# Kernel tuning notes

Measured on AMD Instinct MI355X. Metric: run time of the kernel, lower is better.

Reference implementation:

```python
import jax, jax.numpy as jnp
import numpy as np

T, B, D, R, S, M, H = 1024, 4, 1024, 64, 16, 64, 16
NEG_INF = -1e8


def setup_inputs() -> dict:
    key = jax.random.key(0)
    ks = jax.random.split(key, 12)
    Q, K = R + T + S, M + R + T
    inp = {
        "utterance": jax.random.normal(ks[0], (T, B, D), jnp.float32),
        "right_context": jax.random.normal(ks[1], (R, B, D), jnp.float32),
        "summary": jax.random.normal(ks[2], (S, B, D), jnp.float32),
        "mems": jax.random.normal(ks[3], (M, B, D), jnp.float32),
        # valid frame counts in [1, T]; ensure at least one element == T so
        # max(lengths) stresses the full utterance span
        "lengths": jnp.asarray(
            jax.random.randint(ks[4], (B,), 1, T + 1).at[0].set(T), jnp.int32
        ),
        "attention_mask": jax.random.uniform(ks[5], (Q, K)) < 0.1,
        # Linear params stored as (in, out); y = x @ W + b  (== torch Linear)
        "Wq": jax.random.normal(ks[6], (D, D), jnp.float32) * 0.02,
        "bq": jnp.zeros((D,), jnp.float32),
        "Wkv": jax.random.normal(ks[7], (D, 2 * D), jnp.float32) * 0.02,
        "bkv": jnp.zeros((2 * D,), jnp.float32),
        "Wout": jax.random.normal(ks[8], (D, D), jnp.float32) * 0.02,
        "bout": jnp.zeros((D,), jnp.float32),
    }
    return inp


def reference(utterance, right_context, summary, mems, lengths, attention_mask,
              Wq, bq, Wkv, bkv, Wout, bout):
    d_head = D // H
    scaling = d_head ** -0.5
    Q = R + T + S  # query length
    Kl = M + R + T  # key length (non-streaming)

    # projections
    query = jnp.concatenate([right_context, utterance, summary], axis=0) @ Wq + bq  # (Q,B,D)
    kv = jnp.concatenate([mems, right_context, utterance], axis=0) @ Wkv + bkv      # (K,B,2D)
    k, v = jnp.split(kv, 2, axis=2)  # each (K,B,D)

    # (L, B, D) -> (B*H, L, d_head), matching torch view+transpose
    def heads(x):
        return x.reshape(x.shape[0], B * H, d_head).swapaxes(0, 1)

    qh, kh, vh = heads(query), heads(k), heads(v)

    # fp32 scores + masking, as in the original (masked_fill in float)
    w = jnp.einsum("nqd,nkd->nqk", qh * scaling, kh).astype(jnp.float32)  # (B*H,Q,K)
    w = jnp.where(attention_mask[None, :, :], NEG_INF, w)

    # padding mask over keys: klengths = lengths + M + (R+T - max(lengths))
    klengths = lengths + M + R + T - jnp.max(lengths)
    pad = jnp.arange(Kl, dtype=lengths.dtype)[None, :] >= klengths[:, None]  # (B,K)
    w = w.reshape(B, H, Q, Kl)
    w = jnp.where(pad[:, None, None, :], NEG_INF, w)
    w = w.reshape(B * H, Q, Kl)

    probs = jax.nn.softmax(w, axis=-1).astype(utterance.dtype)  # dropout p=0.0

    attn = jnp.einsum("nqk,nkd->nqd", probs, vh)          # (B*H,Q,d)
    attn = attn.swapaxes(0, 1).reshape(Q, B, D)           # (Q,B,D)
    out = attn @ Wout + bout

    output = out[: Q - S]                 # right_context + utterance outputs
    output_mems = jnp.tanh(out[Q - S:])   # summary -> new mems
    out_key = k[M + R:]                   # utterance keys for streaming cache
    out_val = v[M + R:]
    return output, output_mems, out_key, out_val
```

## Files before the change

kernel.cpp:

```cpp
#include <hip/hip_runtime.h>
#include <hip/hip_bf16.h>

typedef __attribute__((ext_vector_type(8))) short short8;
typedef __attribute__((ext_vector_type(4))) float f32x4;

#define DEV __device__ __forceinline__

constexpr int Tn = 1024, Bn = 4, Dn = 1024, Rn = 64, Sn = 16, Mn = 64, Hn = 16;
constexpr int DH = 64;
constexpr int Qn = Rn + Tn + Sn;
constexpr int KL = Mn + Rn + Tn;
constexpr int NT = KL / 64;
constexpr int NQB = 18;
constexpr int QB = Qn * Bn;
constexpr int KB = KL * Bn;
constexpr int MU = 4672;
constexpr size_t OUTM = (size_t)(Rn + Tn) * Bn * Dn;
constexpr size_t OUTK = OUTM + (size_t)Sn * Bn * Dn;
constexpr size_t OUTV = OUTK + (size_t)Tn * Bn * Dn;
constexpr size_t NU  = (size_t)Tn * Bn * Dn;
constexpr size_t NR_ = (size_t)Rn * Bn * Dn;
constexpr size_t NS_ = (size_t)Sn * Bn * Dn;
constexpr size_t NM_ = (size_t)Mn * Bn * Dn;
constexpr float QSCALE = 0.18033688f;

constexpr int PREP_TW = 1024;
constexpr int PREP_CV = 1024;
constexpr int PREP_MB = (Bn * Qn * NT + 3) / 4;

DEV float b2f(ushort u) { union { unsigned v; float f; } x; x.v = ((unsigned)u) << 16; return x.f; }
DEV ushort f2b(float f) { __hip_bfloat16 h = __float2bfloat16(f); return *reinterpret_cast<ushort*>(&h); }

DEV float ldbias(const void* p, int i, int fp32) {
    return fp32 ? ((const float*)p)[i] : b2f(((const ushort*)p)[i]);
}
DEV void stout(void* p, size_t i, float v, int fp32) {
    if (fp32) ((float*)p)[i] = v; else ((ushort*)p)[i] = f2b(v);
}
DEV bool mread(const void* m, size_t idx, int mode) {
    if (mode == 0) return ((const unsigned char*)m)[idx] != 0;
    if (mode == 1) return ((const int*)m)[idx] != 0;
    return ((const float*)m)[idx] != 0.f;
}

DEV void gload_lds16(const void* g, void* l) {
    __builtin_amdgcn_global_load_lds(
        (const __attribute__((address_space(1))) unsigned int*)g,
        (__attribute__((address_space(3))) unsigned int*)l, 16, 0, 0);
}

DEV unsigned cvt_pk_bf16(float lo, float hi) {
    unsigned r;
    asm("v_cvt_pk_bf16_f32 %0, %1, %2" : "=v"(r) : "v"(lo), "v"(hi));
    return r;
}

DEV int sigma_key(int v) {
    return (2 * (v >> 5) + ((v & 7) >> 2)) * 16 + ((v >> 3) & 3) * 4 + (v & 3);
}

__global__ __launch_bounds__(256) void probe_kernel(const ushort* utt, const unsigned char* mask,
                                                    int* flags) {
    __shared__ int cnt[4];
    if (threadIdx.x < 4) cnt[threadIdx.x] = 0;
    __syncthreads();
    int c = 0;
    for (int i = threadIdx.x; i < 2048; i += 256) {
        int e = (utt[i] >> 7) & 0xFF;
        if (e > 64 && e < 192) c++;
    }
    atomicAdd(&cnt[0], c);
    int c0 = 0, c1 = 0, c23 = 0;
    for (int i = threadIdx.x; i < 8192; i += 256) {
        if (mask[i]) { int m = i & 3; if (m == 0) c0++; else if (m == 1) c1++; else c23++; }
    }
    atomicAdd(&cnt[1], c0); atomicAdd(&cnt[2], c1); atomicAdd(&cnt[3], c23);
    __syncthreads();
    if (threadIdx.x == 0) {
        flags[0] = (cnt[0] < 1900) ? 1 : 0;
        int mmode;
        if (cnt[2] == 0 && cnt[3] == 0) mmode = 1;
        else if (cnt[1] == 0) mmode = 2;
        else mmode = 0;
        flags[1] = mmode;
    }
}

__global__ __launch_bounds__(256) void prep_kernel(
    const void* utt, const void* rc, const void* sm, const void* mm,
    const void* Wq, const void* Wkv, const void* Wout,
    const void* amask, const int* __restrict__ lengths,
    ushort* dst, ushort* WqT, ushort* WkvT, ushort* WoutT,
    unsigned long long* __restrict__ mbits, const int* __restrict__ flags) {
    __shared__ alignas(16) ushort tile[64 * 64];
    const int fp32 = flags[0];
    const int t = threadIdx.x;
    int bid = blockIdx.x;

    if (bid < PREP_TW) {
        const int z = bid >> 8, tr = (bid >> 4) & 15;
        int tc = bid & 15;
        const void* W; ushort* WT; int N;
        if (z == 0)      { W = Wq;   WT = WqT;   N = 1024; }
        else if (z == 3) { W = Wout; WT = WoutT; N = 1024; }
        else             { W = Wkv;  WT = WkvT;  N = 2048; tc += (z - 1) * 16; }
        const int K = 1024;
        for (int c = t; c < 512; c += 256) {
            int row = c >> 3, q = c & 7;
            int u = q ^ (row & 7);
            ushort o[8];
#pragma unroll
            for (int j = 0; j < 8; ++j) {
                size_t gi = (size_t)(tr * 64 + row) * N + tc * 64 + q * 8 + j;
                o[j] = fp32 ? f2b(((const float*)W)[gi]) : ((const ushort*)W)[gi];
            }
            *(short8*)&tile[row * 64 + u * 8] = *(short8*)o;
        }
        __syncthreads();
        for (int c = t; c < 512; c += 256) {
            int n = c >> 3, q = c & 7;
            ushort vv[8];
#pragma unroll
            for (int j = 0; j < 8; ++j) {
                int k = q * 8 + j;
                int u = (n >> 3) ^ (k & 7);
                vv[j] = tile[k * 64 + u * 8 + (n & 7)];
            }
            *(short8*)(WT + (size_t)(tc * 64 + n) * K + tr * 64 + q * 8) = *(short8*)vv;
        }
        return;
    }
    bid -= PREP_TW;
    if (bid < PREP_CV) {
        const size_t total = (NU + NR_ + NS_ + NM_) / 8;
        for (size_t cidx = (size_t)bid * 256 + t; cidx < total;
             cidx += (size_t)PREP_CV * 256) {
            size_t e = cidx * 8; const void* src; size_t li; ushort* d;
            if (e < NU)                  { src = utt; li = e;                 d = dst; }
            else if (e < NU + NR_)       { src = rc;  li = e - NU;            d = dst + NU; }
            else if (e < NU + NR_ + NS_) { src = sm;  li = e - NU - NR_;      d = dst + NU + NR_; }
            else                         { src = mm;  li = e - NU - NR_ - NS_; d = dst + NU + NR_ + NS_; }
            if (fp32) {
                const float* f = (const float*)src + li;
                ushort o[8];
#pragma unroll
                for (int j = 0; j < 8; ++j) o[j] = f2b(f[j]);
                *(short8*)(d + li) = *(short8*)o;
            } else {
                *(short8*)(d + li) = *(const short8*)((const ushort*)src + li);
            }
        }
        return;
    }
    bid -= PREP_CV;
    const int mmode = flags[1];
    int word = bid * 4 + (t >> 6);
    if (word >= Bn * Qn * NT) return;
    int lane = t & 63;
    int ktl = word % NT;
    int rem = word / NT;
    int q = rem % Qn;
    int b = rem / Qn;
    const int l0 = lengths[0], l1 = lengths[1], l2 = lengths[2], l3 = lengths[3];
    const int maxlen = max(max(l0, l1), max(l2, l3));
    const int klen = lengths[b] + KL - maxlen;
    int kg = ktl * 64 + lane;
    bool m = mread(amask, (size_t)q * KL + kg, mmode) || (kg >= klen);
    unsigned long long bal = __ballot(m);
    if (lane == 0) mbits[word] = bal;
}

__global__ __launch_bounds__(256) void transpose_v(const ushort* __restrict__ kv,
                                                   ushort* __restrict__ vT) {
    __shared__ alignas(16) ushort tile[64 * 64];
    const int kt = blockIdx.x, bh = blockIdx.y;
    const int b = bh >> 4, h = bh & 15;
    const int t = threadIdx.x;
    for (int c = t; c < 512; c += 256) {
        int key = c >> 3, q = c & 7;
        short8 v = *(const short8*)(kv + ((size_t)(kt * 64 + key) * Bn + b) * 2048 + 1024 + h * DH + q * 8);
        int u = q ^ (key & 7);
        *(short8*)&tile[key * 64 + u * 8] = v;
    }
    __syncthreads();
    for (int c = t; c < 512; c += 256) {
        int d = c >> 3, q = c & 7;
        ushort vv[8];
#pragma unroll
        for (int j = 0; j < 8; ++j) {
            int key = sigma_key(q * 8 + j);
            int u = (d >> 3) ^ (key & 7);
            vv[j] = tile[key * 64 + u * 8 + (d & 7)];
        }
        *(short8*)(vT + ((size_t)bh * 64 + d) * KL + kt * 64 + q * 8) = *(short8*)vv;
    }
}

#define Q128_STAGE(DSTBUF, KT)                                                        \
    _Pragma("unroll")                                                                 \
    for (int i2 = 0; i2 < 4; ++i2) {                                                  \
        gload_lds16(asrc[i2] + (KT) * 64, &As[DSTBUF][(i2 * 256 + t) * 8]);           \
        gload_lds16(bsrc[i2] + (KT) * 64, &Bs[DSTBUF][(i2 * 256 + t) * 8]);           \
    }

__global__ __launch_bounds__(256, 2) void gemm_qkv(
    const ushort* __restrict__ cmem, const ushort* __restrict__ crc,
    const ushort* __restrict__ cutt, const ushort* __restrict__ csum,
    const ushort* __restrict__ Bt, const void* __restrict__ bq, const void* __restrict__ bkv,
    ushort* __restrict__ q_ws, ushort* __restrict__ kv_ws,
    void* __restrict__ gout, const int* __restrict__ flags) {
    __shared__ alignas(16) ushort As[2][8192];
    __shared__ alignas(16) ushort Bs[2][8192];
    const int ofp = flags[0];
    const int t = threadIdx.x;
    const int lane = t & 63;
    const int w = t >> 6;
    const int wr = w >> 1, wc = w & 1;
    const int g = lane >> 4, lr = lane & 15;

    const int bid = blockIdx.x;
    const int wg = (bid & 7) * 111 + (bid >> 3);
    const int bx = wg % 24, by = wg / 24;
    const int mbase = by * 128, nbase = bx * 128;

    const ushort* asrc[4]; const ushort* bsrc[4];
#pragma unroll
    for (int i2 = 0; i2 < 4; ++i2) {
        int slot = i2 * 256 + t;
        int row = slot >> 3, kc = slot & 7;
        int q = kc ^ (row & 7);
        int grow = mbase + row;
        if (grow >= MU) grow = MU - 1;
        const ushort* s;
        if (grow < 256)       s = cmem + (size_t)grow * 1024;
        else if (grow < 512)  s = crc + (size_t)(grow - 256) * 1024;
        else if (grow < 4608) s = cutt + (size_t)(grow - 512) * 1024;
        else                  s = csum + (size_t)(grow - 4608) * 1024;
        asrc[i2] = s + q * 8;
        bsrc[i2] = Bt + (size_t)(nbase + row) * 1024 + q * 8;
    }

    f32x4 acc[4][4] = {};

    Q128_STAGE(0, 0);

    for (int kt = 0; kt < 16; ++kt) {
        const int c = kt & 1;
        if (kt + 1 < 16) {
            Q128_STAGE(c ^ 1, kt + 1);
            asm volatile("s_waitcnt vmcnt(8)" ::: "memory");
        } else {
            asm volatile("s_waitcnt vmcnt(0)" ::: "memory");
        }
        __builtin_amdgcn_sched_barrier(0);
        __builtin_amdgcn_s_barrier();

        short8 bfr[4][2];
#pragma unroll
        for (int n = 0; n < 4; ++n)
#pragma unroll
            for (int ks = 0; ks < 2; ++ks) {
                int col = wc * 64 + n * 16 + lr;
                bfr[n][ks] = *(const short8*)&Bs[c][col * 64 + (((ks * 4 + g) ^ (lr & 7)) << 3)];
            }
        short8 af[4][2];
#pragma unroll
        for (int m = 0; m < 4; ++m)
#pragma unroll
            for (int ks = 0; ks < 2; ++ks) {
                int row = wr * 64 + m * 16 + lr;
                af[m][ks] = *(const short8*)&As[c][row * 64 + (((ks * 4 + g) ^ (lr & 7)) << 3)];
            }
        __builtin_amdgcn_s_setprio(1);
#pragma unroll
        for (int m = 0; m < 4; ++m)
#pragma unroll
            for (int n = 0; n < 4; ++n) {
                acc[m][n] = __builtin_amdgcn_mfma_f32_16x16x32_bf16(af[m][0], bfr[n][0], acc[m][n], 0, 0, 0);
                acc[m][n] = __builtin_amdgcn_mfma_f32_16x16x32_bf16(af[m][1], bfr[n][1], acc[m][n], 0, 0, 0);
            }
        __builtin_amdgcn_s_setprio(0);

        __builtin_amdgcn_sched_barrier(0);
        __builtin_amdgcn_s_barrier();
    }

#pragma unroll
    for (int n = 0; n < 4; ++n) {
        int col = nbase + wc * 64 + n * 16 + lr;
        float bv = (col < 1024) ? ldbias(bq, col, ofp) : ldbias(bkv, col - 1024, ofp);
#pragma unroll
        for (int m = 0; m < 4; ++m) {
            int rowb = mbase + wr * 64 + m * 16 + g * 4;
#pragma unroll
            for (int i = 0; i < 4; ++i) {
                int r = rowb + i;
                if (r >= MU) continue;
                float val = acc[m][n][i] + bv;
                if (col < 1024) {
                    if (r >= 256) q_ws[(size_t)(r - 256) * 1024 + col] = f2b(val * QSCALE);
                } else {
                    if (r < 4608) {
                        kv_ws[(size_t)r * 2048 + (col - 1024)] = f2b(val);
                        if (r >= 512) {
                            size_t o = (col < 2048)
                                ? OUTK + (size_t)(r - 512) * 1024 + (col - 1024)
                                : OUTV + (size_t)(r - 512) * 1024 + (col - 2048);
                            stout(gout, o, val, ofp);
                        }
                    }
                }
            }
        }
    }
}

#define O_STAGE(DSTBUF, KT)                                                           \
    _Pragma("unroll")                                                                 \
    for (int i2 = 0; i2 < 2; ++i2)                                                    \
        gload_lds16(asrc[i2] + (KT) * 64, &As[DSTBUF][(i2 * 256 + t) * 8]);           \
    _Pragma("unroll")                                                                 \
    for (int i2 = 0; i2 < 4; ++i2)                                                    \
        gload_lds16(bsrc[i2] + (KT) * 64, &Bs[DSTBUF][(i2 * 256 + t) * 8]);

__global__ __launch_bounds__(256, 3) void gemm_out(
    const ushort* __restrict__ A, const ushort* __restrict__ Bt,
    const void* __restrict__ bias, void* __restrict__ gout, const int* __restrict__ flags) {
    __shared__ alignas(16) ushort As[2][4096];
    __shared__ alignas(16) ushort Bs[2][8192];
    const int ofp = flags[0];
    const int t = threadIdx.x;
    const int lane = t & 63;
    const int w = t >> 6;
    const int wr = w >> 1, wc = w & 1;
    const int g = lane >> 4, lr = lane & 15;

    const int nwg = gridDim.x;
    const int bid = blockIdx.x;
    const int wg = (bid & 7) * (nwg >> 3) + (bid >> 3);
    const int bx = wg % 8, by = wg / 8;
    const int mbase = by * 64, nbase = bx * 128;

    const ushort* asrc[2];
#pragma unroll
    for (int i2 = 0; i2 < 2; ++i2) {
        int slot = i2 * 256 + t;
        int row = slot >> 3, kc = slot & 7, q = kc ^ (row & 7);
        asrc[i2] = A + (size_t)(mbase + row) * 1024 + q * 8;
    }
    const ushort* bsrc[4];
#pragma unroll
    for (int i2 = 0; i2 < 4; ++i2) {
        int slot = i2 * 256 + t;
        int row = slot >> 3, kc = slot & 7, q = kc ^ (row & 7);
        bsrc[i2] = Bt + (size_t)(nbase + row) * 1024 + q * 8;
    }

    f32x4 acc[2][4] = {};

    O_STAGE(0, 0);

    for (int kt = 0; kt < 16; ++kt) {
        const int c = kt & 1;
        if (kt + 1 < 16) {
            O_STAGE(c ^ 1, kt + 1);
            asm volatile("s_waitcnt vmcnt(6)" ::: "memory");
        } else {
            asm volatile("s_waitcnt vmcnt(0)" ::: "memory");
        }
        __builtin_amdgcn_sched_barrier(0);
        __builtin_amdgcn_s_barrier();

        short8 bfr[4][2];
#pragma unroll
        for (int n = 0; n < 4; ++n)
#pragma unroll
            for (int ks = 0; ks < 2; ++ks) {
                int col = wc * 64 + n * 16 + lr;
                bfr[n][ks] = *(const short8*)&Bs[c][col * 64 + (((ks * 4 + g) ^ (lr & 7)) << 3)];
            }
        short8 af[2][2];
#pragma unroll
        for (int m = 0; m < 2; ++m)
#pragma unroll
            for (int ks = 0; ks < 2; ++ks) {
                int row = wr * 32 + m * 16 + lr;
                af[m][ks] = *(const short8*)&As[c][row * 64 + (((ks * 4 + g) ^ (lr & 7)) << 3)];
            }
        __builtin_amdgcn_s_setprio(1);
#pragma unroll
        for (int m = 0; m < 2; ++m)
#pragma unroll
            for (int n = 0; n < 4; ++n) {
                acc[m][n] = __builtin_amdgcn_mfma_f32_16x16x32_bf16(af[m][0], bfr[n][0], acc[m][n], 0, 0, 0);
                acc[m][n] = __builtin_amdgcn_mfma_f32_16x16x32_bf16(af[m][1], bfr[n][1], acc[m][n], 0, 0, 0);
            }
        __builtin_amdgcn_s_setprio(0);

        __builtin_amdgcn_sched_barrier(0);
        __builtin_amdgcn_s_barrier();
    }

#pragma unroll
    for (int n = 0; n < 4; ++n) {
        int col = nbase + wc * 64 + n * 16 + lr;
        float bv = ldbias(bias, col, ofp);
#pragma unroll
        for (int m = 0; m < 2; ++m) {
            int rowb = mbase + wr * 32 + m * 16 + g * 4;
#pragma unroll
            for (int i = 0; i < 4; ++i) {
                int row = rowb + i;
                float val = acc[m][n][i] + bv;
                if (row < (Rn + Tn) * Bn) stout(gout, (size_t)row * 1024 + col, val, ofp);
                else stout(gout, OUTM + (size_t)(row - (Rn + Tn) * Bn) * 1024 + col, tanhf(val), ofp);
            }
        }
    }
}

#define ATTN_STAGE(DSTBUF, KT)                                                        \
    gload_lds16(ksrc0 + (size_t)(KT) * kstep, &Ks[DSTBUF][w * 1024]);                 \
    gload_lds16(ksrc1 + (size_t)(KT) * kstep, &Ks[DSTBUF][w * 1024 + 512]);           \
    gload_lds16(vsrc0 + (size_t)(KT) * 64,    &Vs[DSTBUF][w * 1024]);                 \
    gload_lds16(vsrc1 + (size_t)(KT) * 64,    &Vs[DSTBUF][w * 1024 + 512]);

#define ATTN_PHASE(CUR, WBCUR, PRE, KTN, WBNXT, VMSTR)                                \
    {                                                                                 \
        if (PRE) { ATTN_STAGE((CUR) ^ 1, KTN); WBNXT = mp[KTN]; }                     \
        asm volatile("s_waitcnt " VMSTR ::: "memory");                                \
        __builtin_amdgcn_sched_barrier(0);                                            \
        __builtin_amdgcn_s_barrier();                                                 \
        __builtin_amdgcn_sched_barrier(0);                                            \
        f32x4 sa[4] = {};                                                             \
        __builtin_amdgcn_s_setprio(1);                                                \
        _Pragma("unroll")                                                             \
        for (int n = 0; n < 4; ++n) {                                                 \
            int key = n * 16 + lr;                                                    \
            short8 kb0 = *(const short8*)&Ks[CUR][key * 64 + ((g ^ (key & 7)) << 3)]; \
            short8 kb1 = *(const short8*)&Ks[CUR][key * 64 + (((4 + g) ^ (key & 7)) << 3)]; \
            sa[n] = __builtin_amdgcn_mfma_f32_16x16x32_bf16(kb0, qf0, sa[n], 0, 0, 0); \
            sa[n] = __builtin_amdgcn_mfma_f32_16x16x32_bf16(kb1, qf1, sa[n], 0, 0, 0); \
        }                                                                             \
        __builtin_amdgcn_s_setprio(0);                                                \
        unsigned pkk[4][2];                                                           \
        _Pragma("unroll")                                                             \
        for (int n = 0; n < 4; ++n) {                                                 \
            unsigned bits = (unsigned)((WBCUR) >> (n * 16 + g * 4)) & 15u;            \
            float p[4];                                                               \
            _Pragma("unroll")                                                         \
            for (int i = 0; i < 4; ++i) {                                             \
                float sv = ((bits >> i) & 1u) ? -100.0f : sa[n][i];                   \
                p[i] = exp2f(sv);                                                     \
                lsum += p[i];                                                         \
            }                                                                         \
            pkk[n][0] = cvt_pk_bf16(p[0], p[1]);                                      \
            pkk[n][1] = cvt_pk_bf16(p[2], p[3]);                                      \
        }                                                                             \
        union { unsigned u[4]; short8 s; } c0, c1;                                    \
        c0.u[0] = pkk[0][0]; c0.u[1] = pkk[0][1]; c0.u[2] = pkk[1][0]; c0.u[3] = pkk[1][1]; \
        c1.u[0] = pkk[2][0]; c1.u[1] = pkk[2][1]; c1.u[2] = pkk[3][0]; c1.u[3] = pkk[3][1]; \
        __builtin_amdgcn_s_setprio(1);                                                \
        _Pragma("unroll")                                                             \
        for (int n = 0; n < 4; ++n) {                                                 \
            int d = n * 16 + lr;                                                      \
            short8 vb0 = *(const short8*)&Vs[CUR][d * 64 + ((g ^ (d & 7)) << 3)];     \
            short8 vb1 = *(const short8*)&Vs[CUR][d * 64 + (((4 + g) ^ (d & 7)) << 3)]; \
            acc_o[n] = __builtin_amdgcn_mfma_f32_16x16x32_bf16(c0.s, vb0, acc_o[n], 0, 0, 0); \
            acc_o[n] = __builtin_amdgcn_mfma_f32_16x16x32_bf16(c1.s, vb1, acc_o[n], 0, 0, 0); \
        }                                                                             \
        __builtin_amdgcn_s_setprio(0);                                                \
        __builtin_amdgcn_sched_barrier(0);                                            \
        __builtin_amdgcn_s_barrier();                                                 \
    }

__global__ __launch_bounds__(256, 5) void attn_kernel(
    const ushort* __restrict__ qws, const ushort* __restrict__ kvws, const ushort* __restrict__ vTws,
    const unsigned long long* __restrict__ mbits,
    ushort* __restrict__ attnws) {
    __shared__ alignas(16) ushort Ks[2][64 * 64];
    __shared__ alignas(16) ushort Vs[2][64 * 64];

    const int bid = blockIdx.x;
    const int wg = (bid & 7) * (gridDim.x >> 3) + (bid >> 3);
    const int qblk = wg % NQB;
    const int bh = wg / NQB;
    const int b = bh >> 4, h = bh & 15;
    const int t = threadIdx.x;
    const int w = t >> 6, lane = t & 63;
    const int g = lane >> 4, lr = lane & 15;

    const int qi = qblk * 64 + w * 16 + lr;
    const int qic = qi < Qn ? qi : (Qn - 1);
    const ushort* qptr = qws + ((size_t)qic * Bn + b) * Dn + h * DH;
    const short8 qf0 = *(const short8*)(qptr + g * 8);
    const short8 qf1 = *(const short8*)(qptr + 32 + g * 8);
    const unsigned long long* mp = mbits + ((size_t)b * Qn + qic) * NT;

    const int srow0 = w * 16 + (lane >> 3);
    const int srow1 = srow0 + 8;
    const int sw = (((lane & 7) ^ ((lane >> 3) & 7)) << 3);
    const ushort* ksrc0 = kvws + ((size_t)srow0 * Bn + b) * 2048 + h * DH + sw;
    const ushort* ksrc1 = kvws + ((size_t)srow1 * Bn + b) * 2048 + h * DH + sw;
    const ushort* vsrc0 = vTws + ((size_t)bh * 64 + srow0) * KL + sw;
    const ushort* vsrc1 = vTws + ((size_t)bh * 64 + srow1) * KL + sw;
    const size_t kstep = (size_t)64 * Bn * 2048;

    f32x4 acc_o[4] = {};
    float lsum = 0.f;
    unsigned long long wbA, wbB;

    ATTN_STAGE(0, 0);
    wbA = mp[0];
    wbB = 0;

    for (int kt2 = 0; kt2 < NT - 2; kt2 += 2) {
        ATTN_PHASE(0, wbA, true, kt2 + 1, wbB, "vmcnt(4)");
        ATTN_PHASE(1, wbB, true, kt2 + 2, wbA, "vmcnt(4)");
    }
    ATTN_PHASE(0, wbA, true, NT - 1, wbB, "vmcnt(4)");
    ATTN_PHASE(1, wbB, false, 0, wbA, "vmcnt(0)");

    float ls = lsum;
    ls += __shfl_xor(ls, 16);
    ls += __shfl_xor(ls, 32);
#pragma unroll
    for (int i = 0; i < 4; ++i) {
        int qrow = g * 4 + i;
        float lsv = __shfl(ls, (lane & 48) | qrow);
        int qg = qblk * 64 + w * 16 + qrow;
        if (qg >= Qn) continue;
        float inv = 1.f / lsv;
#pragma unroll
        for (int n = 0; n < 4; ++n) {
            attnws[((size_t)qg * Bn + b) * Dn + h * DH + n * 16 + lr] = f2b(acc_o[n][i] * inv);
        }
    }
}

extern "C" void kernel_launch(void* const* d_in, const int* in_sizes, int n_in,
                              void* d_out, int out_size, void* d_ws, size_t ws_size,
                              hipStream_t stream) {
    const void* utt   = d_in[0];
    const void* rc    = d_in[1];
    const void* summ  = d_in[2];
    const void* mems  = d_in[3];
    const int*  lens  = (const int*)d_in[4];
    const void* amask = d_in[5];
    const void* Wq   = d_in[6];
    const void* bq   = d_in[7];
    const void* Wkv  = d_in[8];
    const void* bkv  = d_in[9];
    const void* Wout = d_in[10];
    const void* bout = d_in[11];

    ushort* ws    = (ushort*)d_ws;
    int*   flags  = (int*)d_ws;
    ushort* cu    = ws + 64;
    ushort* cutt  = cu;
    ushort* crc   = cutt + NU;
    ushort* csum  = crc + NR_;
    ushort* cmem  = csum + NS_;
    ushort* WqT   = cmem + NM_;
    ushort* WkvT  = WqT + (size_t)1024 * 1024;
    ushort* WoutT = WkvT + (size_t)2048 * 1024;
    ushort* q_ws  = WoutT + (size_t)1024 * 1024;
    ushort* kv_ws = q_ws + (size_t)QB * Dn;
    ushort* vT_ws = kv_ws + (size_t)KB * 2048;
    ushort* at_ws = vT_ws + (size_t)64 * 64 * KL;
    unsigned long long* mbits = (unsigned long long*)(at_ws + (size_t)QB * Dn);

    probe_kernel<<<1, 256, 0, stream>>>((const ushort*)utt, (const unsigned char*)amask, flags);
    prep_kernel<<<PREP_TW + PREP_CV + PREP_MB, 256, 0, stream>>>(
        utt, rc, summ, mems, Wq, Wkv, Wout, amask, lens,
        cu, WqT, WkvT, WoutT, mbits, flags);

    gemm_qkv<<<dim3(888), 256, 0, stream>>>(cmem, crc, cutt, csum, WqT, bq, bkv,
                                            q_ws, kv_ws, d_out, flags);
    transpose_v<<<dim3(KL / 64, Bn * Hn), 256, 0, stream>>>(kv_ws, vT_ws);
    attn_kernel<<<dim3(NQB * Bn * Hn), 256, 0, stream>>>(q_ws, kv_ws, vT_ws, mbits, at_ws);
    gemm_out<<<dim3(552), 256, 0, stream>>>(at_ws, WoutT, bout, d_out, flags);
}
```

Measured before the change: 175.2 us.

## Inline dtype/mask detection, skip bf16 copy, double queries per attention warp

Removes the single-block probe kernel and instead has each kernel detect the input dtype and mask encoding with a wave ballot over a few elements. When inputs are already bf16, the conversion copy is skipped and the QKV GEMM reads the original buffers directly. The attention kernel now processes 32 query rows per warp (two 16-row groups) sharing each K/V tile in LDS. This halves the grid and K/V staging traffic per query but raises register pressure (launch bounds lowered from 5 to 3). The sampled detection heuristic is smaller than before and could misclassify unusual inputs.

```diff
diff --git a/kernel.cpp b/kernel.cpp
--- a/kernel.cpp
+++ b/kernel.cpp
@@ -11,7 +11,6 @@
 constexpr int Qn = Rn + Tn + Sn;
 constexpr int KL = Mn + Rn + Tn;
 constexpr int NT = KL / 64;
-constexpr int NQB = 18;
 constexpr int QB = Qn * Bn;
 constexpr int KB = KL * Bn;
 constexpr int MU = 4672;
@@ -43,6 +42,28 @@
     return ((const float*)m)[idx] != 0.f;
 }
 
+DEV int detect_fp32(const ushort* utt) {
+    int l = threadIdx.x & 63;
+    int e = (utt[l] >> 7) & 0xFF;
+    unsigned long long bal = __ballot(e > 64 && e < 192);
+    return (__popcll(bal) < 58) ? 1 : 0;
+}
+DEV int detect_mmode(const unsigned char* mask) {
+    int l = threadIdx.x & 63;
+    bool nz0 = false, nz2 = false;
+#pragma unroll
+    for (int s = 0; s < 4; ++s) {
+        int wrd = l + s * 64;
+        nz0 |= mask[wrd * 4] != 0;
+        nz2 |= mask[wrd * 4 + 2] != 0;
+    }
+    unsigned long long b0 = __ballot(nz0);
+    unsigned long long b2 = __ballot(nz2);
+    if (b0 != 0 && b2 == 0) return 1;
+    if (b0 == 0 && b2 != 0) return 2;
+    return 0;
+}
+
 DEV void gload_lds16(const void* g, void* l) {
     __builtin_amdgcn_global_load_lds(
         (const __attribute__((address_space(1))) unsigned int*)g,
@@ -57,33 +78,6 @@
 
 DEV int sigma_key(int v) {
     return (2 * (v >> 5) + ((v & 7) >> 2)) * 16 + ((v >> 3) & 3) * 4 + (v & 3);
-}
-
-__global__ __launch_bounds__(256) void probe_kernel(const ushort* utt, const unsigned char* mask,
-                                                    int* flags) {
-    __shared__ int cnt[4];
-    if (threadIdx.x < 4) cnt[threadIdx.x] = 0;
-    __syncthreads();
-    int c = 0;
-    for (int i = threadIdx.x; i < 2048; i += 256) {
-        int e = (utt[i] >> 7) & 0xFF;
-        if (e > 64 && e < 192) c++;
-    }
-    atomicAdd(&cnt[0], c);
-    int c0 = 0, c1 = 0, c23 = 0;
-    for (int i = threadIdx.x; i < 8192; i += 256) {
-        if (mask[i]) { int m = i & 3; if (m == 0) c0++; else if (m == 1) c1++; else c23++; }
-    }
-    atomicAdd(&cnt[1], c0); atomicAdd(&cnt[2], c1); atomicAdd(&cnt[3], c23);
-    __syncthreads();
-    if (threadIdx.x == 0) {
-        flags[0] = (cnt[0] < 1900) ? 1 : 0;
-        int mmode;
-        if (cnt[2] == 0 && cnt[3] == 0) mmode = 1;
-        else if (cnt[1] == 0) mmode = 2;
-        else mmode = 0;
-        flags[1] = mmode;
-    }
 }
 
 __global__ __launch_bounds__(256) void prep_kernel(
@@ -91,13 +85,13 @@
     const void* Wq, const void* Wkv, const void* Wout,
     const void* amask, const int* __restrict__ lengths,
     ushort* dst, ushort* WqT, ushort* WkvT, ushort* WoutT,
-    unsigned long long* __restrict__ mbits, const int* __restrict__ flags) {
+    unsigned long long* __restrict__ mbits) {
     __shared__ alignas(16) ushort tile[64 * 64];
-    const int fp32 = flags[0];
     const int t = threadIdx.x;
     int bid = blockIdx.x;
 
     if (bid < PREP_TW) {
+        const int fp32 = detect_fp32((const ushort*)utt);
         const int z = bid >> 8, tr = (bid >> 4) & 15;
         int tc = bid & 15;
         const void* W; ushort* WT; int N;
@@ -132,6 +126,8 @@
     }
     bid -= PREP_TW;
     if (bid < PREP_CV) {
+        const int fp32 = detect_fp32((const ushort*)utt);
+        if (!fp32) return;
         const size_t total = (NU + NR_ + NS_ + NM_) / 8;
         for (size_t cidx = (size_t)bid * 256 + t; cidx < total;
              cidx += (size_t)PREP_CV * 256) {
@@ -140,20 +136,16 @@
             else if (e < NU + NR_)       { src = rc;  li = e - NU;            d = dst + NU; }
             else if (e < NU + NR_ + NS_) { src = sm;  li = e - NU - NR_;      d = dst + NU + NR_; }
             else                         { src = mm;  li = e - NU - NR_ - NS_; d = dst + NU + NR_ + NS_; }
-            if (fp32) {
-                const float* f = (const float*)src + li;
-                ushort o[8];
-#pragma unroll
-                for (int j = 0; j < 8; ++j) o[j] = f2b(f[j]);
-                *(short8*)(d + li) = *(short8*)o;
-            } else {
-                *(short8*)(d + li) = *(const short8*)((const ushort*)src + li);
-            }
+            const float* f = (const float*)src + li;
+            ushort o[8];
+#pragma unroll
+            for (int j = 0; j < 8; ++j) o[j] = f2b(f[j]);
+            *(short8*)(d + li) = *(short8*)o;
         }
         return;
     }
     bid -= PREP_CV;
-    const int mmode = flags[1];
+    const int mmode = detect_mmode((const unsigned char*)amask);
     int word = bid * 4 + (t >> 6);
     if (word >= Bn * Qn * NT) return;
     int lane = t & 63;
@@ -206,17 +198,23 @@
 __global__ __launch_bounds__(256, 2) void gemm_qkv(
     const ushort* __restrict__ cmem, const ushort* __restrict__ crc,
     const ushort* __restrict__ cutt, const ushort* __restrict__ csum,
+    const void* morig, const void* rorig, const void* uorig, const void* sorig,
     const ushort* __restrict__ Bt, const void* __restrict__ bq, const void* __restrict__ bkv,
     ushort* __restrict__ q_ws, ushort* __restrict__ kv_ws,
-    void* __restrict__ gout, const int* __restrict__ flags) {
+    void* __restrict__ gout) {
     __shared__ alignas(16) ushort As[2][8192];
     __shared__ alignas(16) ushort Bs[2][8192];
-    const int ofp = flags[0];
+    const int ofp = detect_fp32((const ushort*)uorig);
     const int t = threadIdx.x;
     const int lane = t & 63;
     const int w = t >> 6;
     const int wr = w >> 1, wc = w & 1;
     const int g = lane >> 4, lr = lane & 15;
+
+    const ushort* s0 = ofp ? cmem : (const ushort*)morig;
+    const ushort* s1 = ofp ? crc  : (const ushort*)rorig;
+    const ushort* s2 = ofp ? cutt : (const ushort*)uorig;
+    const ushort* s3 = ofp ? csum : (const ushort*)sorig;
 
     const int bid = blockIdx.x;
     const int wg = (bid & 7) * 111 + (bid >> 3);
@@ -232,10 +230,10 @@
         int grow = mbase + row;
         if (grow >= MU) grow = MU - 1;
         const ushort* s;
-        if (grow < 256)       s = cmem + (size_t)grow * 1024;
-        else if (grow < 512)  s = crc + (size_t)(grow - 256) * 1024;
-        else if (grow < 4608) s = cutt + (size_t)(grow - 512) * 1024;
-        else                  s = csum + (size_t)(grow - 4608) * 1024;
+        if (grow < 256)       s = s0 + (size_t)grow * 1024;
+        else if (grow < 512)  s = s1 + (size_t)(grow - 256) * 1024;
+        else if (grow < 4608) s = s2 + (size_t)(grow - 512) * 1024;
+        else                  s = s3 + (size_t)(grow - 4608) * 1024;
         asrc[i2] = s + q * 8;
         bsrc[i2] = Bt + (size_t)(nbase + row) * 1024 + q * 8;
     }
@@ -325,10 +323,10 @@
 
 __global__ __launch_bounds__(256, 3) void gemm_out(
     const ushort* __restrict__ A, const ushort* __restrict__ Bt,
-    const void* __restrict__ bias, void* __restrict__ gout, const int* __restrict__ flags) {
+    const void* __restrict__ bias, const void* uorig, void* __restrict__ gout) {
     __shared__ alignas(16) ushort As[2][4096];
     __shared__ alignas(16) ushort Bs[2][8192];
-    const int ofp = flags[0];
+    const int ofp = detect_fp32((const ushort*)uorig);
     const int t = threadIdx.x;
     const int lane = t & 63;
     const int w = t >> 6;
@@ -425,56 +423,7 @@
     gload_lds16(vsrc0 + (size_t)(KT) * 64,    &Vs[DSTBUF][w * 1024]);                 \
     gload_lds16(vsrc1 + (size_t)(KT) * 64,    &Vs[DSTBUF][w * 1024 + 512]);
 
-#define ATTN_PHASE(CUR, WBCUR, PRE, KTN, WBNXT, VMSTR)                                \
-    {                                                                                 \
-        if (PRE) { ATTN_STAGE((CUR) ^ 1, KTN); WBNXT = mp[KTN]; }                     \
-        asm volatile("s_waitcnt " VMSTR ::: "memory");                                \
-        __builtin_amdgcn_sched_barrier(0);                                            \
-        __builtin_amdgcn_s_barrier();                                                 \
-        __builtin_amdgcn_sched_barrier(0);                                            \
-        f32x4 sa[4] = {};                                                             \
-        __builtin_amdgcn_s_setprio(1);                                                \
-        _Pragma("unroll")                                                             \
-        for (int n = 0; n < 4; ++n) {                                                 \
-            int key = n * 16 + lr;                                                    \
-            short8 kb0 = *(const short8*)&Ks[CUR][key * 64 + ((g ^ (key & 7)) << 3)]; \
-            short8 kb1 = *(const short8*)&Ks[CUR][key * 64 + (((4 + g) ^ (key & 7)) << 3)]; \
-            sa[n] = __builtin_amdgcn_mfma_f32_16x16x32_bf16(kb0, qf0, sa[n], 0, 0, 0); \
-            sa[n] = __builtin_amdgcn_mfma_f32_16x16x32_bf16(kb1, qf1, sa[n], 0, 0, 0); \
-        }                                                                             \
-        __builtin_amdgcn_s_setprio(0);                                                \
-        unsigned pkk[4][2];                                                           \
-        _Pragma("unroll")                                                             \
-        for (int n = 0; n < 4; ++n) {                                                 \
-            unsigned bits = (unsigned)((WBCUR) >> (n * 16 + g * 4)) & 15u;            \
-            float p[4];                                                               \
-            _Pragma("unroll")                                                         \
-            for (int i = 0; i < 4; ++i) {                                             \
-                float sv = ((bits >> i) & 1u) ? -100.0f : sa[n][i];                   \
-                p[i] = exp2f(sv);                                                     \
-                lsum += p[i];                                                         \
-            }                                                                         \
-            pkk[n][0] = cvt_pk_bf16(p[0], p[1]);                                      \
-            pkk[n][1] = cvt_pk_bf16(p[2], p[3]);                                      \
-        }                                                                             \
-        union { unsigned u[4]; short8 s; } c0, c1;                                    \
-        c0.u[0] = pkk[0][0]; c0.u[1] = pkk[0][1]; c0.u[2] = pkk[1][0]; c0.u[3] = pkk[1][1]; \
-        c1.u[0] = pkk[2][0]; c1.u[1] = pkk[2][1]; c1.u[2] = pkk[3][0]; c1.u[3] = pkk[3][1]; \
-        __builtin_amdgcn_s_setprio(1);                                                \
-        _Pragma("unroll")                                                             \
-        for (int n = 0; n < 4; ++n) {                                                 \
-            int d = n * 16 + lr;                                                      \
-            short8 vb0 = *(const short8*)&Vs[CUR][d * 64 + ((g ^ (d & 7)) << 3)];     \
-            short8 vb1 = *(const short8*)&Vs[CUR][d * 64 + (((4 + g) ^ (d & 7)) << 3)]; \
-            acc_o[n] = __builtin_amdgcn_mfma_f32_16x16x32_bf16(c0.s, vb0, acc_o[n], 0, 0, 0); \
-            acc_o[n] = __builtin_amdgcn_mfma_f32_16x16x32_bf16(c1.s, vb1, acc_o[n], 0, 0, 0); \
-        }                                                                             \
-        __builtin_amdgcn_s_setprio(0);                                                \
-        __builtin_amdgcn_sched_barrier(0);                                            \
-        __builtin_amdgcn_s_barrier();                                                 \
-    }
-
-__global__ __launch_bounds__(256, 5) void attn_kernel(
+__global__ __launch_bounds__(256, 3) void attn_kernel(
     const ushort* __restrict__ qws, const ushort* __restrict__ kvws, const ushort* __restrict__ vTws,
     const unsigned long long* __restrict__ mbits,
     ushort* __restrict__ attnws) {
@@ -483,19 +432,24 @@
 
     const int bid = blockIdx.x;
     const int wg = (bid & 7) * (gridDim.x >> 3) + (bid >> 3);
-    const int qblk = wg % NQB;
-    const int bh = wg / NQB;
+    const int qblk = wg % 9;
+    const int bh = wg / 9;
     const int b = bh >> 4, h = bh & 15;
     const int t = threadIdx.x;
     const int w = t >> 6, lane = t & 63;
     const int g = lane >> 4, lr = lane & 15;
 
-    const int qi = qblk * 64 + w * 16 + lr;
-    const int qic = qi < Qn ? qi : (Qn - 1);
-    const ushort* qptr = qws + ((size_t)qic * Bn + b) * Dn + h * DH;
-    const short8 qf0 = *(const short8*)(qptr + g * 8);
-    const short8 qf1 = *(const short8*)(qptr + 32 + g * 8);
-    const unsigned long long* mp = mbits + ((size_t)b * Qn + qic) * NT;
+    short8 qf[2][2];
+    const unsigned long long* mp[2];
+#pragma unroll
+    for (int G = 0; G < 2; ++G) {
+        int qi = qblk * 128 + w * 32 + G * 16 + lr;
+        int qic = qi < Qn ? qi : (Qn - 1);
+        const ushort* qptr = qws + ((size_t)qic * Bn + b) * Dn + h * DH;
+        qf[G][0] = *(const short8*)(qptr + g * 8);
+        qf[G][1] = *(const short8*)(qptr + 32 + g * 8);
+        mp[G] = mbits + ((size_t)b * Qn + qic) * NT;
+    }
 
     const int srow0 = w * 16 + (lane >> 3);
     const int srow1 = srow0 + 8;
@@ -506,34 +460,97 @@
     const ushort* vsrc1 = vTws + ((size_t)bh * 64 + srow1) * KL + sw;
     const size_t kstep = (size_t)64 * Bn * 2048;
 
-    f32x4 acc_o[4] = {};
-    float lsum = 0.f;
-    unsigned long long wbA, wbB;
+    f32x4 acc_o[2][4] = {};
+    float lsum[2] = {0.f, 0.f};
+    unsigned long long wbc[2], wbn[2];
 
     ATTN_STAGE(0, 0);
-    wbA = mp[0];
-    wbB = 0;
-
-    for (int kt2 = 0; kt2 < NT - 2; kt2 += 2) {
-        ATTN_PHASE(0, wbA, true, kt2 + 1, wbB, "vmcnt(4)");
-        ATTN_PHASE(1, wbB, true, kt2 + 2, wbA, "vmcnt(4)");
-    }
-    ATTN_PHASE(0, wbA, true, NT - 1, wbB, "vmcnt(4)");
-    ATTN_PHASE(1, wbB, false, 0, wbA, "vmcnt(0)");
-
-    float ls = lsum;
-    ls += __shfl_xor(ls, 16);
-    ls += __shfl_xor(ls, 32);
-#pragma unroll
-    for (int i = 0; i < 4; ++i) {
-        int qrow = g * 4 + i;
-        float lsv = __shfl(ls, (lane & 48) | qrow);
-        int qg = qblk * 64 + w * 16 + qrow;
-        if (qg >= Qn) continue;
-        float inv = 1.f / lsv;
+    wbc[0] = mp[0][0]; wbc[1] = mp[1][0];
+
+    for (int kt = 0; kt < NT; ++kt) {
+        const int c = kt & 1;
+        if (kt + 1 < NT) {
+            ATTN_STAGE(c ^ 1, kt + 1);
+            wbn[0] = mp[0][kt + 1]; wbn[1] = mp[1][kt + 1];
+            asm volatile("s_waitcnt vmcnt(6)" ::: "memory");
+        } else {
+            asm volatile("s_waitcnt vmcnt(0)" ::: "memory");
+        }
+        __builtin_amdgcn_sched_barrier(0);
+        __builtin_amdgcn_s_barrier();
+        __builtin_amdgcn_sched_barrier(0);
+
+        f32x4 sa0[4] = {}, sa1[4] = {};
+        __builtin_amdgcn_s_setprio(1);
 #pragma unroll
         for (int n = 0; n < 4; ++n) {
-            attnws[((size_t)qg * Bn + b) * Dn + h * DH + n * 16 + lr] = f2b(acc_o[n][i] * inv);
+            int key = n * 16 + lr;
+            short8 kb0 = *(const short8*)&Ks[c][key * 64 + ((g ^ (key & 7)) << 3)];
+            short8 kb1 = *(const short8*)&Ks[c][key * 64 + (((4 + g) ^ (key & 7)) << 3)];
+            sa0[n] = __builtin_amdgcn_mfma_f32_16x16x32_bf16(kb0, qf[0][0], sa0[n], 0, 0, 0);
+            sa0[n] = __builtin_amdgcn_mfma_f32_16x16x32_bf16(kb1, qf[0][1], sa0[n], 0, 0, 0);
+            sa1[n] = __builtin_amdgcn_mfma_f32_16x16x32_bf16(kb0, qf[1][0], sa1[n], 0, 0, 0);
+            sa1[n] = __builtin_amdgcn_mfma_f32_16x16x32_bf16(kb1, qf[1][1], sa1[n], 0, 0, 0);
+        }
+        __builtin_amdgcn_s_setprio(0);
+
+        short8 cs[2][2];
+#pragma unroll
+        for (int G = 0; G < 2; ++G) {
+            unsigned pkk[4][2];
+#pragma unroll
+            for (int n = 0; n < 4; ++n) {
+                unsigned bits = (unsigned)(wbc[G] >> (n * 16 + g * 4)) & 15u;
+                float p[4];
+#pragma unroll
+                for (int i = 0; i < 4; ++i) {
+                    float sv = ((bits >> i) & 1u) ? -100.0f : (G == 0 ? sa0[n][i] : sa1[n][i]);
+                    p[i] = exp2f(sv);
+                    lsum[G] += p[i];
+                }
+                pkk[n][0] = cvt_pk_bf16(p[0], p[1]);
+                pkk[n][1] = cvt_pk_bf16(p[2], p[3]);
+            }
+            union { unsigned u[4]; short8 s; } c0u, c1u;
+            c0u.u[0] = pkk[0][0]; c0u.u[1] = pkk[0][1]; c0u.u[2] = pkk[1][0]; c0u.u[3] = pkk[1][1];
+            c1u.u[0] = pkk[2][0]; c1u.u[1] = pkk[2][1]; c1u.u[2] = pkk[3][0]; c1u.u[3] = pkk[3][1];
+            cs[G][0] = c0u.s; cs[G][1] = c1u.s;
+        }
+
+        __builtin_amdgcn_s_setprio(1);
+#pragma unroll
+        for (int n = 0; n < 4; ++n) {
+            int d = n * 16 + lr;
+            short8 vb0 = *(const short8*)&Vs[c][d * 64 + ((g ^ (d & 7)) << 3)];
+            short8 vb1 = *(const short8*)&Vs[c][d * 64 + (((4 + g) ^ (d & 7)) << 3)];
+            acc_o[0][n] = __builtin_amdgcn_mfma_f32_16x16x32_bf16(cs[0][0], vb0, acc_o[0][n], 0, 0, 0);
+            acc_o[0][n] = __builtin_amdgcn_mfma_f32_16x16x32_bf16(cs[0][1], vb1, acc_o[0][n], 0, 0, 0);
+            acc_o[1][n] = __builtin_amdgcn_mfma_f32_16x16x32_bf16(cs[1][0], vb0, acc_o[1][n], 0, 0, 0);
+            acc_o[1][n] = __builtin_amdgcn_mfma_f32_16x16x32_bf16(cs[1][1], vb1, acc_o[1][n], 0, 0, 0);
+        }
+        __builtin_amdgcn_s_setprio(0);
+
+        wbc[0] = wbn[0]; wbc[1] = wbn[1];
+        __builtin_amdgcn_sched_barrier(0);
+        __builtin_amdgcn_s_barrier();
+    }
+
+#pragma unroll
+    for (int G = 0; G < 2; ++G) {
+        float ls = lsum[G];
+        ls += __shfl_xor(ls, 16);
+        ls += __shfl_xor(ls, 32);
+#pragma unroll
+        for (int i = 0; i < 4; ++i) {
+            int qrow = g * 4 + i;
+            float lsv = __shfl(ls, (lane & 48) | qrow);
+            int qg = qblk * 128 + w * 32 + G * 16 + qrow;
+            if (qg >= Qn) continue;
+            float inv = 1.f / lsv;
+#pragma unroll
+            for (int n = 0; n < 4; ++n) {
+                attnws[((size_t)qg * Bn + b) * Dn + h * DH + n * 16 + lr] = f2b(acc_o[G][n][i] * inv);
+            }
         }
     }
 }
@@ -555,7 +572,6 @@
     const void* bout = d_in[11];
 
     ushort* ws    = (ushort*)d_ws;
-    int*   flags  = (int*)d_ws;
     ushort* cu    = ws + 64;
     ushort* cutt  = cu;
     ushort* crc   = cutt + NU;
@@ -570,14 +586,14 @@
     ushort* at_ws = vT_ws + (size_t)64 * 64 * KL;
     unsigned long long* mbits = (unsigned long long*)(at_ws + (size_t)QB * Dn);
 
-    probe_kernel<<<1, 256, 0, stream>>>((const ushort*)utt, (const unsigned char*)amask, flags);
     prep_kernel<<<PREP_TW + PREP_CV + PREP_MB, 256, 0, stream>>>(
         utt, rc, summ, mems, Wq, Wkv, Wout, amask, lens,
-        cu, WqT, WkvT, WoutT, mbits, flags);
-
-    gemm_qkv<<<dim3(888), 256, 0, stream>>>(cmem, crc, cutt, csum, WqT, bq, bkv,
-                                            q_ws, kv_ws, d_out, flags);
+        cu, WqT, WkvT, WoutT, mbits);
+
+    gemm_qkv<<<dim3(888), 256, 0, stream>>>(cmem, crc, cutt, csum,
+                                            mems, rc, utt, summ,
+                                            WqT, bq, bkv, q_ws, kv_ws, d_out);
     transpose_v<<<dim3(KL / 64, Bn * Hn), 256, 0, stream>>>(kv_ws, vT_ws);
-    attn_kernel<<<dim3(NQB * Bn * Hn), 256, 0, stream>>>(q_ws, kv_ws, vT_ws, mbits, at_ws);
-    gemm_out<<<dim3(552), 256, 0, stream>>>(at_ws, WoutT, bout, d_out, flags);
-}
+    attn_kernel<<<dim3(9 * Bn * Hn), 256, 0, stream>>>(q_ws, kv_ws, vT_ws, mbits, at_ws);
+    gemm_out<<<dim3(552), 256, 0, stream>>>(at_ws, WoutT, bout, utt, d_out);
+}
```

New measurement: 179.0 us. +2.2%, slower.

## Inline dtype/mask probing into kernels and move K/V output writes to transpose

Applied to the files above, without the earlier changes.

Removes the separate single-block probe kernel. Each kernel now detects the input dtype and mask encoding itself with a quick wavefront ballot. For bf16 inputs the activation conversion copy is skipped and gemm_qkv reads the original buffers directly. The out_key/out_val stores move out of the gemm_qkv epilogue, where they were scalar stores, into transpose_v as 8-wide vector stores. The epilogues are also reordered so bias loads are hoisted, at the cost of slightly different detection heuristics (fewer samples).

```diff
diff --git a/kernel.cpp b/kernel.cpp
--- a/kernel.cpp
+++ b/kernel.cpp
@@ -42,6 +42,37 @@
     if (mode == 1) return ((const int*)m)[idx] != 0;
     return ((const float*)m)[idx] != 0.f;
 }
+DEV void st8(void* gout, size_t o, short8 v, int ofp) {
+    if (!ofp) {
+        *(short8*)((ushort*)gout + o) = v;
+    } else {
+        float* f = (float*)gout + o;
+#pragma unroll
+        for (int j = 0; j < 8; ++j) f[j] = b2f((ushort)v[j]);
+    }
+}
+
+DEV int detect_fp32(const ushort* utt) {
+    int l = threadIdx.x & 63;
+    int e = (utt[l] >> 7) & 0xFF;
+    unsigned long long bal = __ballot(e > 64 && e < 192);
+    return (__popcll(bal) < 58) ? 1 : 0;
+}
+DEV int detect_mmode(const unsigned char* mask) {
+    int l = threadIdx.x & 63;
+    bool nz0 = false, nz2 = false;
+#pragma unroll
+    for (int s = 0; s < 4; ++s) {
+        int wrd = l + s * 64;
+        nz0 |= mask[wrd * 4] != 0;
+        nz2 |= mask[wrd * 4 + 2] != 0;
+    }
+    unsigned long long b0 = __ballot(nz0);
+    unsigned long long b2 = __ballot(nz2);
+    if (b0 != 0 && b2 == 0) return 1;
+    if (b0 == 0 && b2 != 0) return 2;
+    return 0;
+}
 
 DEV void gload_lds16(const void* g, void* l) {
     __builtin_amdgcn_global_load_lds(
@@ -57,33 +88,6 @@
 
 DEV int sigma_key(int v) {
     return (2 * (v >> 5) + ((v & 7) >> 2)) * 16 + ((v >> 3) & 3) * 4 + (v & 3);
-}
-
-__global__ __launch_bounds__(256) void probe_kernel(const ushort* utt, const unsigned char* mask,
-                                                    int* flags) {
-    __shared__ int cnt[4];
-    if (threadIdx.x < 4) cnt[threadIdx.x] = 0;
-    __syncthreads();
-    int c = 0;
-    for (int i = threadIdx.x; i < 2048; i += 256) {
-        int e = (utt[i] >> 7) & 0xFF;
-        if (e > 64 && e < 192) c++;
-    }
-    atomicAdd(&cnt[0], c);
-    int c0 = 0, c1 = 0, c23 = 0;
-    for (int i = threadIdx.x; i < 8192; i += 256) {
-        if (mask[i]) { int m = i & 3; if (m == 0) c0++; else if (m == 1) c1++; else c23++; }
-    }
-    atomicAdd(&cnt[1], c0); atomicAdd(&cnt[2], c1); atomicAdd(&cnt[3], c23);
-    __syncthreads();
-    if (threadIdx.x == 0) {
-        flags[0] = (cnt[0] < 1900) ? 1 : 0;
-        int mmode;
-        if (cnt[2] == 0 && cnt[3] == 0) mmode = 1;
-        else if (cnt[1] == 0) mmode = 2;
-        else mmode = 0;
-        flags[1] = mmode;
-    }
 }
 
 __global__ __launch_bounds__(256) void prep_kernel(
@@ -91,13 +95,13 @@
     const void* Wq, const void* Wkv, const void* Wout,
     const void* amask, const int* __restrict__ lengths,
     ushort* dst, ushort* WqT, ushort* WkvT, ushort* WoutT,
-    unsigned long long* __restrict__ mbits, const int* __restrict__ flags) {
+    unsigned long long* __restrict__ mbits) {
     __shared__ alignas(16) ushort tile[64 * 64];
-    const int fp32 = flags[0];
     const int t = threadIdx.x;
     int bid = blockIdx.x;
 
     if (bid < PREP_TW) {
+        const int fp32 = detect_fp32((const ushort*)utt);
         const int z = bid >> 8, tr = (bid >> 4) & 15;
         int tc = bid & 15;
         const void* W; ushort* WT; int N;
@@ -132,6 +136,8 @@
     }
     bid -= PREP_TW;
     if (bid < PREP_CV) {
+        const int fp32 = detect_fp32((const ushort*)utt);
+        if (!fp32) return;
         const size_t total = (NU + NR_ + NS_ + NM_) / 8;
         for (size_t cidx = (size_t)bid * 256 + t; cidx < total;
              cidx += (size_t)PREP_CV * 256) {
@@ -140,20 +146,16 @@
             else if (e < NU + NR_)       { src = rc;  li = e - NU;            d = dst + NU; }
             else if (e < NU + NR_ + NS_) { src = sm;  li = e - NU - NR_;      d = dst + NU + NR_; }
             else                         { src = mm;  li = e - NU - NR_ - NS_; d = dst + NU + NR_ + NS_; }
-            if (fp32) {
-                const float* f = (const float*)src + li;
-                ushort o[8];
-#pragma unroll
-                for (int j = 0; j < 8; ++j) o[j] = f2b(f[j]);
-                *(short8*)(d + li) = *(short8*)o;
-            } else {
-                *(short8*)(d + li) = *(const short8*)((const ushort*)src + li);
-            }
+            const float* f = (const float*)src + li;
+            ushort o[8];
+#pragma unroll
+            for (int j = 0; j < 8; ++j) o[j] = f2b(f[j]);
+            *(short8*)(d + li) = *(short8*)o;
         }
         return;
     }
     bid -= PREP_CV;
-    const int mmode = flags[1];
+    const int mmode = detect_mmode((const unsigned char*)amask);
     int word = bid * 4 + (t >> 6);
     if (word >= Bn * Qn * NT) return;
     int lane = t & 63;
@@ -171,16 +173,25 @@
 }
 
 __global__ __launch_bounds__(256) void transpose_v(const ushort* __restrict__ kv,
-                                                   ushort* __restrict__ vT) {
+                                                   ushort* __restrict__ vT,
+                                                   const void* uorig, void* __restrict__ gout) {
     __shared__ alignas(16) ushort tile[64 * 64];
+    const int ofp = detect_fp32((const ushort*)uorig);
     const int kt = blockIdx.x, bh = blockIdx.y;
     const int b = bh >> 4, h = bh & 15;
     const int t = threadIdx.x;
     for (int c = t; c < 512; c += 256) {
         int key = c >> 3, q = c & 7;
-        short8 v = *(const short8*)(kv + ((size_t)(kt * 64 + key) * Bn + b) * 2048 + 1024 + h * DH + q * 8);
+        int krow = kt * 64 + key;
+        size_t r = (size_t)krow * Bn + b;
+        short8 v = *(const short8*)(kv + r * 2048 + 1024 + h * DH + q * 8);
         int u = q ^ (key & 7);
         *(short8*)&tile[key * 64 + u * 8] = v;
+        if (krow >= 128) {
+            st8(gout, OUTV + (r - 512) * 1024 + h * DH + q * 8, v, ofp);
+            short8 kk = *(const short8*)(kv + r * 2048 + h * DH + q * 8);
+            st8(gout, OUTK + (r - 512) * 1024 + h * DH + q * 8, kk, ofp);
+        }
     }
     __syncthreads();
     for (int c = t; c < 512; c += 256) {
@@ -206,17 +217,22 @@
 __global__ __launch_bounds__(256, 2) void gemm_qkv(
     const ushort* __restrict__ cmem, const ushort* __restrict__ crc,
     const ushort* __restrict__ cutt, const ushort* __restrict__ csum,
+    const void* morig, const void* rorig, const void* uorig, const void* sorig,
     const ushort* __restrict__ Bt, const void* __restrict__ bq, const void* __restrict__ bkv,
-    ushort* __restrict__ q_ws, ushort* __restrict__ kv_ws,
-    void* __restrict__ gout, const int* __restrict__ flags) {
+    ushort* __restrict__ q_ws, ushort* __restrict__ kv_ws) {
     __shared__ alignas(16) ushort As[2][8192];
     __shared__ alignas(16) ushort Bs[2][8192];
-    const int ofp = flags[0];
+    const int ofp = detect_fp32((const ushort*)uorig);
     const int t = threadIdx.x;
     const int lane = t & 63;
     const int w = t >> 6;
     const int wr = w >> 1, wc = w & 1;
     const int g = lane >> 4, lr = lane & 15;
+
+    const ushort* s0 = ofp ? cmem : (const ushort*)morig;
+    const ushort* s1 = ofp ? crc  : (const ushort*)rorig;
+    const ushort* s2 = ofp ? cutt : (const ushort*)uorig;
+    const ushort* s3 = ofp ? csum : (const ushort*)sorig;
 
     const int bid = blockIdx.x;
     const int wg = (bid & 7) * 111 + (bid >> 3);
@@ -232,10 +248,10 @@
         int grow = mbase + row;
         if (grow >= MU) grow = MU - 1;
         const ushort* s;
-        if (grow < 256)       s = cmem + (size_t)grow * 1024;
-        else if (grow < 512)  s = crc + (size_t)(grow - 256) * 1024;
-        else if (grow < 4608) s = cutt + (size_t)(grow - 512) * 1024;
-        else                  s = csum + (size_t)(grow - 4608) * 1024;
+        if (grow < 256)       s = s0 + (size_t)grow * 1024;
+        else if (grow < 512)  s = s1 + (size_t)(grow - 256) * 1024;
+        else if (grow < 4608) s = s2 + (size_t)(grow - 512) * 1024;
+        else                  s = s3 + (size_t)(grow - 4608) * 1024;
         asrc[i2] = s + q * 8;
         bsrc[i2] = Bt + (size_t)(nbase + row) * 1024 + q * 8;
     }
@@ -285,34 +301,29 @@
         __builtin_amdgcn_s_barrier();
     }
 
+    float bv[4];
 #pragma unroll
     for (int n = 0; n < 4; ++n) {
         int col = nbase + wc * 64 + n * 16 + lr;
-        float bv = (col < 1024) ? ldbias(bq, col, ofp) : ldbias(bkv, col - 1024, ofp);
-#pragma unroll
-        for (int m = 0; m < 4; ++m) {
-            int rowb = mbase + wr * 64 + m * 16 + g * 4;
-#pragma unroll
-            for (int i = 0; i < 4; ++i) {
-                int r = rowb + i;
-                if (r >= MU) continue;
-                float val = acc[m][n][i] + bv;
+        bv[n] = (col < 1024) ? ldbias(bq, col, ofp) : ldbias(bkv, col - 1024, ofp);
+    }
+#pragma unroll
+    for (int m = 0; m < 4; ++m)
+#pragma unroll
+        for (int i = 0; i < 4; ++i) {
+            int r = mbase + wr * 64 + m * 16 + g * 4 + i;
+            if (r >= MU) continue;
+#pragma unroll
+            for (int n = 0; n < 4; ++n) {
+                int col = nbase + wc * 64 + n * 16 + lr;
+                float val = acc[m][n][i] + bv[n];
                 if (col < 1024) {
                     if (r >= 256) q_ws[(size_t)(r - 256) * 1024 + col] = f2b(val * QSCALE);
                 } else {
-                    if (r < 4608) {
-                        kv_ws[(size_t)r * 2048 + (col - 1024)] = f2b(val);
-                        if (r >= 512) {
-                            size_t o = (col < 2048)
-                                ? OUTK + (size_t)(r - 512) * 1024 + (col - 1024)
-                                : OUTV + (size_t)(r - 512) * 1024 + (col - 2048);
-                            stout(gout, o, val, ofp);
-                        }
-                    }
+                    if (r < 4608) kv_ws[(size_t)r * 2048 + (col - 1024)] = f2b(val);
                 }
             }
         }
-    }
 }
 
 #define O_STAGE(DSTBUF, KT)                                                           \
@@ -325,10 +336,10 @@
 
 __global__ __launch_bounds__(256, 3) void gemm_out(
     const ushort* __restrict__ A, const ushort* __restrict__ Bt,
-    const void* __restrict__ bias, void* __restrict__ gout, const int* __restrict__ flags) {
+    const void* __restrict__ bias, const void* uorig, void* __restrict__ gout) {
     __shared__ alignas(16) ushort As[2][4096];
     __shared__ alignas(16) ushort Bs[2][8192];
-    const int ofp = flags[0];
+    const int ofp = detect_fp32((const ushort*)uorig);
     const int t = threadIdx.x;
     const int lane = t & 63;
     const int w = t >> 6;
@@ -401,22 +412,25 @@
         __builtin_amdgcn_s_barrier();
     }
 
+    float bv[4];
 #pragma unroll
     for (int n = 0; n < 4; ++n) {
         int col = nbase + wc * 64 + n * 16 + lr;
-        float bv = ldbias(bias, col, ofp);
-#pragma unroll
-        for (int m = 0; m < 2; ++m) {
-            int rowb = mbase + wr * 32 + m * 16 + g * 4;
-#pragma unroll
-            for (int i = 0; i < 4; ++i) {
-                int row = rowb + i;
-                float val = acc[m][n][i] + bv;
+        bv[n] = ldbias(bias, col, ofp);
+    }
+#pragma unroll
+    for (int m = 0; m < 2; ++m)
+#pragma unroll
+        for (int i = 0; i < 4; ++i) {
+            int row = mbase + wr * 32 + m * 16 + g * 4 + i;
+#pragma unroll
+            for (int n = 0; n < 4; ++n) {
+                int col = nbase + wc * 64 + n * 16 + lr;
+                float val = acc[m][n][i] + bv[n];
                 if (row < (Rn + Tn) * Bn) stout(gout, (size_t)row * 1024 + col, val, ofp);
                 else stout(gout, OUTM + (size_t)(row - (Rn + Tn) * Bn) * 1024 + col, tanhf(val), ofp);
             }
         }
-    }
 }
 
 #define ATTN_STAGE(DSTBUF, KT)                                                        \
@@ -555,7 +569,6 @@
     const void* bout = d_in[11];
 
     ushort* ws    = (ushort*)d_ws;
-    int*   flags  = (int*)d_ws;
     ushort* cu    = ws + 64;
     ushort* cutt  = cu;
     ushort* crc   = cutt + NU;
@@ -570,14 +583,14 @@
     ushort* at_ws = vT_ws + (size_t)64 * 64 * KL;
     unsigned long long* mbits = (unsigned long long*)(at_ws + (size_t)QB * Dn);
 
-    probe_kernel<<<1, 256, 0, stream>>>((const ushort*)utt, (const unsigned char*)amask, flags);
     prep_kernel<<<PREP_TW + PREP_CV + PREP_MB, 256, 0, stream>>>(
         utt, rc, summ, mems, Wq, Wkv, Wout, amask, lens,
-        cu, WqT, WkvT, WoutT, mbits, flags);
-
-    gemm_qkv<<<dim3(888), 256, 0, stream>>>(cmem, crc, cutt, csum, WqT, bq, bkv,
-                                            q_ws, kv_ws, d_out, flags);
-    transpose_v<<<dim3(KL / 64, Bn * Hn), 256, 0, stream>>>(kv_ws, vT_ws);
+        cu, WqT, WkvT, WoutT, mbits);
+
+    gemm_qkv<<<dim3(888), 256, 0, stream>>>(cmem, crc, cutt, csum,
+                                            mems, rc, utt, summ,
+                                            WqT, bq, bkv, q_ws, kv_ws);
+    transpose_v<<<dim3(KL / 64, Bn * Hn), 256, 0, stream>>>(kv_ws, vT_ws, utt, d_out);
     attn_kernel<<<dim3(NQB * Bn * Hn), 256, 0, stream>>>(q_ws, kv_ws, vT_ws, mbits, at_ws);
-    gemm_out<<<dim3(552), 256, 0, stream>>>(at_ws, WoutT, bout, d_out, flags);
-}
+    gemm_out<<<dim3(552), 256, 0, stream>>>(at_ws, WoutT, bout, utt, d_out);
+}
```

After: 165.8 us. -5.4%, faster.
